# Optimization experiments

Hardware: AMD Instinct MI355X
Metric: run time of the kernel (lower is better)

Reference implementation:

```python
import jax, jax.numpy as jnp
import numpy as np

D_MODEL = 256
B, H, T = 4, 8, 2048
EPS = 1e-8


def _clinear(x_r, x_i, w_r, w_i, b_r, b_i):
    # complex matmul: (x_r + i x_i) @ (w_r + i w_i)^T + (b_r + i b_i)
    y_r = jnp.matmul(x_r, w_r.T) - jnp.matmul(x_i, w_i.T) + b_r
    y_i = jnp.matmul(x_i, w_r.T) + jnp.matmul(x_r, w_i.T) + b_i
    return y_r, y_i


def setup_inputs() -> dict:
    key = jax.random.key(0)
    ks = jax.random.split(key, 24)
    d = D_MODEL
    std = np.sqrt(2.0 / (d + d)) / np.sqrt(2.0)  # glorot-ish * 1/sqrt(2) as in _init_weights
    inp = {}
    inp['q_in_r'] = jax.random.normal(ks[0], (B, H, T, d), jnp.float32)
    inp['q_in_i'] = jax.random.normal(ks[1], (B, H, T, d), jnp.float32)
    inp['kv_in_r'] = jax.random.normal(ks[2], (B, H, T, d), jnp.float32)
    inp['kv_in_i'] = jax.random.normal(ks[3], (B, H, T, d), jnp.float32)
    i = 4
    for p in ['q', 'k', 'v', 'o']:
        inp[p + '_wr'] = std * jax.random.normal(ks[i], (d, d), jnp.float32); i += 1
        inp[p + '_wi'] = std * jax.random.normal(ks[i], (d, d), jnp.float32); i += 1
        inp[p + '_br'] = jnp.zeros((d,), jnp.float32)
        inp[p + '_bi'] = jnp.zeros((d,), jnp.float32)
    inp['gate_w'] = std * jax.random.normal(ks[i], (d, d), jnp.float32)
    inp['gate_b'] = jnp.zeros((d,), jnp.float32)
    return inp


def reference(q_in_r, q_in_i, kv_in_r, kv_in_i,
              q_wr, q_wi, q_br, q_bi,
              k_wr, k_wi, k_br, k_bi,
              v_wr, v_wi, v_br, v_bi,
              o_wr, o_wi, o_br, o_bi,
              gate_w, gate_b):
    D = q_in_r.shape[-1]
    q_r, q_i = _clinear(q_in_r, q_in_i, q_wr, q_wi, q_br, q_bi)
    k_r, k_i = _clinear(kv_in_r, kv_in_i, k_wr, k_wi, k_br, k_bi)
    v_r, v_i = _clinear(kv_in_r, kv_in_i, v_wr, v_wi, v_br, v_bi)
    scale = 1.0 / np.sqrt(D)
    # real part of complex inner product <q, k> (the module's dual-part score)
    scores = (jnp.einsum('bhqd,bhkd->bhqk', q_r, k_r)
              + jnp.einsum('bhqd,bhkd->bhqk', q_i, k_i)) * scale
    attn = jax.nn.softmax(scores, axis=-1)
    ctx_r = jnp.einsum('bhqk,bhkd->bhqd', attn, v_r)
    ctx_i = jnp.einsum('bhqk,bhkd->bhqd', attn, v_i)
    out_r, out_i = _clinear(ctx_r, ctx_i, o_wr, o_wi, o_br, o_bi)
    out_mag = jnp.sqrt(out_r ** 2 + out_i ** 2 + EPS)
    gate = jax.nn.sigmoid(jnp.matmul(out_mag, gate_w.T) + gate_b)
    return out_r * gate, out_i * gate
```

## Files before the change

kernel.cpp:

```cpp
#include <hip/hip_runtime.h>
#include <hip/hip_bf16.h>
#include <hip/hip_fp16.h>
#include <stdint.h>


#define TSEQ   2048
#define NHEADS 32
#define MTOT   65536
#define DDC    512
#define HCHUNK 8

typedef float    f32x4  __attribute__((ext_vector_type(4)));
typedef _Float16 f16x8  __attribute__((ext_vector_type(8)));
typedef uint16_t u16x4  __attribute__((ext_vector_type(4)));
typedef uint16_t u16x8  __attribute__((ext_vector_type(8)));

__device__ __forceinline__ uint16_t f2h(float f) {
  _Float16 h = (_Float16)f;
  return __builtin_bit_cast(uint16_t, h);
}
__device__ __forceinline__ float h2f(uint16_t u) {
  return (float)__builtin_bit_cast(_Float16, u);
}

__device__ __forceinline__ void gld16(const void* g, void* l) {
  __builtin_amdgcn_global_load_lds(
      (const __attribute__((address_space(1))) uint32_t*)g,
      (__attribute__((address_space(3))) uint32_t*)l, 16, 0, 0);
}

enum { EP_F16Z = 0, EP_PROJ = 1, EP_OUT = 2, EP_GATE = 3 };

template <int EP, int BM>
__global__ __launch_bounds__(512, (BM == 128) ? 4 : 2) void gemm_bt(
    const uint16_t* __restrict__ A, int lda, long zA,
    const uint16_t* __restrict__ B, int ldb, long zB,
    void* __restrict__ C, int ldc, long zC, uint16_t* __restrict__ CV,
    int K,
    const float* __restrict__ biasR, const float* __restrict__ biasI,
    float scale, float* __restrict__ outR, float* __restrict__ outI) {
  constexpr int MI    = BM / 32;
  constexpr int ASLAB = BM / 64;
  constexpr int ABUFE = BM * 64;
  constexpr int BUFE  = (BM + 256) * 64;
  constexpr int NLOAD = ASLAB + 4;
  __shared__ uint16_t lds[2 * BUFE];

  const int tid  = threadIdx.x;
  const int wave = tid >> 6;
  const int lane = tid & 63;
  const int wr   = (wave >> 2) * (BM / 2);
  const int wc   = (wave & 3) * 64;

  const int gx = gridDim.x, gy = gridDim.y;
  const int nwg = gx * gy * gridDim.z;
  const int lin = blockIdx.x + gx * (blockIdx.y + gy * blockIdx.z);
  const int cpx = nwg >> 3;
  const int swz = (lin & 7) * cpx + (lin >> 3);
  const int shx = __popc(gx - 1);
  const int shy = __popc(gy - 1);
  const int bx = swz & (gx - 1);
  const int by = (swz >> shx) & (gy - 1);
  const int bz = swz >> (shx + shy);

  const long tm = (long)by * BM;
  const long tn = (long)bx * 256;
  const uint16_t* Ab = A + (long)bz * zA;
  const uint16_t* Bb = B + (long)bz * zB;

  f32x4 acc[MI][4] = {};

  const int arow   = wave * 8 + (lane >> 3);
  const int schunk = (lane & 7) ^ (lane >> 3);

  const int fr   = lane & 15;
  const int quad = lane >> 4;
  const int sw   = fr & 7;
  const int ch0  = ((0 + quad) ^ sw) * 16;
  const int ch1  = ((4 + quad) ^ sw) * 16;

  const int nt = K >> 6;

  auto STAGE = [&](int buf, int t) {
    const long k0 = (long)t * 64 + schunk * 8;
    uint16_t* base = lds + buf * BUFE;
#pragma unroll
    for (int s = 0; s < ASLAB; ++s)
      gld16(Ab + (tm + s * 64 + arow) * (long)lda + k0,
            base + (s * 64 + wave * 8) * 64);
#pragma unroll
    for (int s = 0; s < 4; ++s)
      gld16(Bb + (tn + s * 64 + arow) * (long)ldb + k0,
            base + ABUFE + (s * 64 + wave * 8) * 64);
  };

  auto COMPUTE = [&](int buf) {
    const char* Abase = (const char*)(lds + buf * BUFE);
    const char* Bbase = Abase + 2 * ABUFE;
#pragma unroll
    for (int ks = 0; ks < 2; ++ks) {
      const int co = ks ? ch1 : ch0;
      f16x8 bf[4];
#pragma unroll
      for (int j = 0; j < 4; ++j)
        bf[j] = *(const f16x8*)(Bbase + (wc + j * 16 + fr) * 128 + co);
#pragma unroll
      for (int i = 0; i < MI; ++i) {
        const f16x8 af = *(const f16x8*)(Abase + (wr + i * 16 + fr) * 128 + co);
#pragma unroll
        for (int j = 0; j < 4; ++j)
          acc[i][j] = __builtin_amdgcn_mfma_f32_16x16x32_f16(af, bf[j], acc[i][j], 0, 0, 0);
      }
    }
  };

  STAGE(0, 0);
  int cur = 0;
  for (int t = 0; t < nt; ++t) {
    if (t + 1 < nt) {
      STAGE(cur ^ 1, t + 1);
      if constexpr (NLOAD == 8)      asm volatile("s_waitcnt vmcnt(8)" ::: "memory");
      else if constexpr (NLOAD == 6) asm volatile("s_waitcnt vmcnt(6)" ::: "memory");
      else                           asm volatile("s_waitcnt vmcnt(0)" ::: "memory");
    } else {
      asm volatile("s_waitcnt vmcnt(0)" ::: "memory");
    }
    __builtin_amdgcn_s_barrier();
    __builtin_amdgcn_sched_barrier(0);
    COMPUTE(cur);
    __builtin_amdgcn_sched_barrier(0);
    __builtin_amdgcn_s_barrier();
    __builtin_amdgcn_sched_barrier(0);
    cur ^= 1;
  }

  if constexpr (EP == EP_F16Z || EP == EP_PROJ) {
    __syncthreads();
    char* wbase = (char*)lds + wave * (BM * 64);
    uint16_t* Cp;
    int coff = 0;
    if constexpr (EP == EP_PROJ) {
      const bool vhalf = (CV != nullptr) && (tn >= 512);
      Cp = vhalf ? CV : (uint16_t*)C;
      coff = vhalf ? 512 : 0;
    } else {
      Cp = (uint16_t*)C + (long)bz * zC;
    }
#pragma unroll
    for (int i = 0; i < MI; ++i) {
#pragma unroll
      for (int j = 0; j < 4; ++j) {
#pragma unroll
        for (int r = 0; r < 4; ++r) {
          const int row = i * 16 + quad * 4 + r;
          int byte = row * 128 + (j * 16 + fr) * 2;
          byte ^= ((row >> 2) & 3) << 5;
          float v = acc[i][j][r];
          if constexpr (EP == EP_PROJ) {
            const int col = (int)tn + wc + j * 16 + fr;
            v += biasR[col];
          } else {
            v *= scale;
          }
          *(uint16_t*)(wbase + byte) = f2h(v);
        }
      }
    }
    asm volatile("s_waitcnt lgkmcnt(0)" ::: "memory");
    __builtin_amdgcn_sched_barrier(0);
#pragma unroll
    for (int it = 0; it < BM / 16; ++it) {
      const int row = it * 8 + (lane >> 3);
      const int c   = lane & 7;
      int byte = row * 128 + c * 16;
      byte ^= ((row >> 2) & 3) << 5;
      const u16x8 val = *(const u16x8*)(wbase + byte);
      const long grow = tm + wr + row;
      const int  gcol = (int)tn + wc + c * 8 - coff;
      *(u16x8*)(Cp + grow * (long)ldc + gcol) = val;
    }
  } else {
#pragma unroll
    for (int i = 0; i < MI; ++i) {
      const long row0 = tm + wr + i * 16 + quad * 4;
#pragma unroll
      for (int j = 0; j < 4; ++j) {
        const int col = (int)tn + wc + j * 16 + fr;
#pragma unroll
        for (int r = 0; r < 4; ++r) {
          float v = acc[i][j][r];
          const long rw = row0 + r;
          if constexpr (EP == EP_OUT) {
            if (col < 256) outR[rw * 256 + col]       = v + biasR[col];
            else           outI[rw * 256 + col - 256] = v + biasI[col - 256];
          } else {
            const float g = 1.0f / (1.0f + __expf(-(v + biasR[col])));
            const long o = rw * 256 + col;
            outR[o] *= g;
            outI[o] *= g;
          }
        }
      }
    }
  }
}

__global__ void pack_x(const float* __restrict__ xr, const float* __restrict__ xi,
                       uint16_t* __restrict__ out) {
  const long idx = (long)blockIdx.x * 256 + threadIdx.x;
  const long m  = idx >> 7;
  const int  c4 = (int)(idx & 127) << 2;
  const float* src = (c4 < 256) ? (xr + m * 256 + c4) : (xi + m * 256 + (c4 - 256));
  const float4 v = *(const float4*)src;
  u16x4 o = {f2h(v.x), f2h(v.y), f2h(v.z), f2h(v.w)};
  *(u16x4*)(out + m * 512 + c4) = o;
}

__global__ void pack_w(const float* __restrict__ wr, const float* __restrict__ wi,
                       uint16_t* __restrict__ out) {
  const int idx = blockIdx.x * 256 + threadIdx.x;
  const int j  = idx >> 7;
  const int c4 = (idx & 127) << 2;
  const float* src;
  float sgn = 1.f;
  if (j < 256) {
    if (c4 < 256) src = wr + j * 256 + c4;
    else { src = wi + j * 256 + (c4 - 256); sgn = -1.f; }
  } else {
    if (c4 < 256) src = wi + (j - 256) * 256 + c4;
    else          src = wr + (j - 256) * 256 + (c4 - 256);
  }
  const float4 v = *(const float4*)src;
  u16x4 o = {f2h(sgn * v.x), f2h(sgn * v.y), f2h(sgn * v.z), f2h(sgn * v.w)};
  *(u16x4*)(out + (long)j * 512 + c4) = o;
}

__global__ void pack_gw(const float* __restrict__ w, uint16_t* __restrict__ out) {
  const int idx = blockIdx.x * 256 + threadIdx.x;
  const float4 v = *(const float4*)(w + (long)idx * 4);
  u16x4 o = {f2h(v.x), f2h(v.y), f2h(v.z), f2h(v.w)};
  *(u16x4*)(out + (long)idx * 4) = o;
}

__global__ void pack_bias(const float* __restrict__ qbr, const float* __restrict__ qbi,
                          const float* __restrict__ kbr, const float* __restrict__ kbi,
                          const float* __restrict__ vbr, const float* __restrict__ vbi,
                          float* __restrict__ bq, float* __restrict__ bkv) {
  const int i = blockIdx.x * 256 + threadIdx.x;
  if (i < 256)       bq[i] = qbr[i];
  else if (i < 512)  bq[i] = qbi[i - 256];
  else if (i < 768)  bkv[i - 512] = kbr[i - 512];
  else if (i < 1024) bkv[i - 512] = kbi[i - 768];
  else if (i < 1280) bkv[i - 512] = vbr[i - 1024];
  else               bkv[i - 512] = vbi[i - 1280];
}

__global__ void transpose_v(const uint16_t* __restrict__ V, uint16_t* __restrict__ Vt) {
  __shared__ uint16_t t[32][33];
  const int h = blockIdx.z;
  const uint16_t* Vh = V + (long)h * TSEQ * DDC;
  uint16_t* Vth = Vt + (long)h * DDC * TSEQ;
  const int t0 = blockIdx.x * 32;
  const int n0 = blockIdx.y * 32;
  const int lx = threadIdx.x & 31, ly = threadIdx.x >> 5;
#pragma unroll
  for (int yy = ly; yy < 32; yy += 8)
    t[yy][lx] = Vh[(long)(t0 + yy) * DDC + n0 + lx];
  __syncthreads();
#pragma unroll
  for (int yy = ly; yy < 32; yy += 8)
    Vth[(long)(n0 + yy) * TSEQ + t0 + lx] = t[lx][yy];
}

__global__ __launch_bounds__(256) void softmax_rows(uint16_t* __restrict__ S) {
  const long row = blockIdx.x;
  uint16_t* p = S + row * 2048;
  const int tid = threadIdx.x;
  u16x8 raw = ((const u16x8*)p)[tid];
  float v[8];
#pragma unroll
  for (int j = 0; j < 8; ++j) v[j] = h2f(raw[j]);
  float m = v[0];
#pragma unroll
  for (int j = 1; j < 8; ++j) m = fmaxf(m, v[j]);
#pragma unroll
  for (int off = 32; off >= 1; off >>= 1) m = fmaxf(m, __shfl_xor(m, off));
  __shared__ float red[8];
  const int wave = tid >> 6, lane = tid & 63;
  if (lane == 0) red[wave] = m;
  __syncthreads();
  m = fmaxf(fmaxf(red[0], red[1]), fmaxf(red[2], red[3]));
  float s = 0.f;
#pragma unroll
  for (int j = 0; j < 8; ++j) { v[j] = __expf(v[j] - m); s += v[j]; }
#pragma unroll
  for (int off = 32; off >= 1; off >>= 1) s += __shfl_xor(s, off);
  if (lane == 0) red[4 + wave] = s;
  __syncthreads();
  s = red[4] + red[5] + red[6] + red[7];
  const float inv = 1.0f / s;
  u16x8 o;
#pragma unroll
  for (int j = 0; j < 8; ++j) o[j] = f2h(v[j] * inv);
  ((u16x8*)p)[tid] = o;
}

__global__ void mag_kernel(const float* __restrict__ R, const float* __restrict__ I,
                           uint16_t* __restrict__ mag) {
  const long i = ((long)blockIdx.x * 256 + threadIdx.x) * 4;
  const float4 r  = *(const float4*)(R + i);
  const float4 im = *(const float4*)(I + i);
  u16x4 o = {f2h(sqrtf(r.x * r.x + im.x * im.x + 1e-8f)),
             f2h(sqrtf(r.y * r.y + im.y * im.y + 1e-8f)),
             f2h(sqrtf(r.z * r.z + im.z * im.z + 1e-8f)),
             f2h(sqrtf(r.w * r.w + im.w * im.w + 1e-8f))};
  *(u16x4*)(mag + i) = o;
}

extern "C" void kernel_launch(void* const* d_in, const int* in_sizes, int n_in,
                              void* d_out, int out_size, void* d_ws, size_t ws_size,
                              hipStream_t stream) {
  const float* q_in_r  = (const float*)d_in[0];
  const float* q_in_i  = (const float*)d_in[1];
  const float* kv_in_r = (const float*)d_in[2];
  const float* kv_in_i = (const float*)d_in[3];
  const float* q_wr = (const float*)d_in[4];
  const float* q_wi = (const float*)d_in[5];
  const float* q_br = (const float*)d_in[6];
  const float* q_bi = (const float*)d_in[7];
  const float* k_wr = (const float*)d_in[8];
  const float* k_wi = (const float*)d_in[9];
  const float* k_br = (const float*)d_in[10];
  const float* k_bi = (const float*)d_in[11];
  const float* v_wr = (const float*)d_in[12];
  const float* v_wi = (const float*)d_in[13];
  const float* v_br = (const float*)d_in[14];
  const float* v_bi = (const float*)d_in[15];
  const float* o_wr = (const float*)d_in[16];
  const float* o_wi = (const float*)d_in[17];
  const float* o_br = (const float*)d_in[18];
  const float* o_bi = (const float*)d_in[19];
  const float* gate_w = (const float*)d_in[20];
  const float* gate_b = (const float*)d_in[21];

  unsigned char* w = (unsigned char*)d_ws;
  const size_t MAT16 = (size_t)MTOT * DDC * 2;
  size_t off = 0;
  uint16_t* R1 = (uint16_t*)(w + off); off += MAT16;
  uint16_t* R2 = (uint16_t*)(w + off); off += MAT16;
  uint16_t* R3 = (uint16_t*)(w + off); off += MAT16;
  uint16_t* R4 = (uint16_t*)(w + off); off += MAT16;
  uint16_t* R5 = (uint16_t*)(w + off); off += MAT16;
  uint16_t* Wq = (uint16_t*)(w + off); off += 512 * 512 * 2;
  uint16_t* Wk = (uint16_t*)(w + off); off += 512 * 512 * 2;
  uint16_t* Wv = (uint16_t*)(w + off); off += 512 * 512 * 2;
  uint16_t* Wo = (uint16_t*)(w + off); off += 512 * 512 * 2;
  uint16_t* Gw = (uint16_t*)(w + off); off += 256 * 256 * 2;
  float*    Bq  = (float*)(w + off);   off += 512 * 4;
  float*    Bkv = (float*)(w + off);   off += 1024 * 4;

  uint16_t* Xq  = R1; uint16_t* Vt  = R1;
  uint16_t* Xkv = R2; uint16_t* Ctx = R2;
  uint16_t* Qm  = R3; uint16_t* Mag = R3;
  uint16_t* Km  = R4;
  uint16_t* Vm  = R5; uint16_t* Sc  = R5;

  float* outR = (float*)d_out;
  float* outI = (float*)d_out + (long)MTOT * 256;

  pack_x<<<32768, 256, 0, stream>>>(q_in_r, q_in_i, Xq);
  pack_x<<<32768, 256, 0, stream>>>(kv_in_r, kv_in_i, Xkv);
  pack_w<<<256, 256, 0, stream>>>(q_wr, q_wi, Wq);
  pack_w<<<256, 256, 0, stream>>>(k_wr, k_wi, Wk);
  pack_w<<<256, 256, 0, stream>>>(v_wr, v_wi, Wv);
  pack_w<<<256, 256, 0, stream>>>(o_wr, o_wi, Wo);
  pack_gw<<<64, 256, 0, stream>>>(gate_w, Gw);
  pack_bias<<<6, 256, 0, stream>>>(q_br, q_bi, k_br, k_bi, v_br, v_bi, Bq, Bkv);

  gemm_bt<EP_PROJ, 256><<<dim3(2, 256, 1), 512, 0, stream>>>(
      Xq, 512, 0, Wq, 512, 0, Qm, 512, 0, nullptr, 512, Bq, nullptr, 1.f,
      nullptr, nullptr);
  gemm_bt<EP_PROJ, 256><<<dim3(4, 256, 1), 512, 0, stream>>>(
      Xkv, 512, 0, Wk, 512, 0, Km, 512, 0, Vm, 512, Bkv, nullptr, 1.f,
      nullptr, nullptr);
  transpose_v<<<dim3(64, 16, 32), 256, 0, stream>>>(Vm, Vt);

  for (int c = 0; c < NHEADS / HCHUNK; ++c) {
    const long ho = (long)c * HCHUNK;
    gemm_bt<EP_F16Z, 256><<<dim3(8, 8, HCHUNK), 512, 0, stream>>>(
        Qm + ho * TSEQ * DDC, 512, (long)TSEQ * DDC,
        Km + ho * TSEQ * DDC, 512, (long)TSEQ * DDC,
        Sc, TSEQ, (long)TSEQ * TSEQ, nullptr, 512,
        nullptr, nullptr, 0.0625f, nullptr, nullptr);
    softmax_rows<<<HCHUNK * TSEQ, 256, 0, stream>>>(Sc);
    gemm_bt<EP_F16Z, 128><<<dim3(2, 16, HCHUNK), 512, 0, stream>>>(
        Sc, TSEQ, (long)TSEQ * TSEQ,
        Vt + ho * DDC * TSEQ, TSEQ, (long)DDC * TSEQ,
        Ctx + ho * TSEQ * DDC, 512, (long)TSEQ * DDC, nullptr, 2048,
        nullptr, nullptr, 1.f, nullptr, nullptr);
  }

  gemm_bt<EP_OUT, 256><<<dim3(2, 256, 1), 512, 0, stream>>>(
      Ctx, 512, 0, Wo, 512, 0, nullptr, 0, 0, nullptr, 512,
      o_br, o_bi, 1.f, outR, outI);

  mag_kernel<<<16384, 256, 0, stream>>>(outR, outI, Mag);

  gemm_bt<EP_GATE, 256><<<dim3(1, 256, 1), 512, 0, stream>>>(
      Mag, 256, 0, Gw, 256, 0, nullptr, 0, 0, nullptr, 256,
      gate_b, nullptr, 1.f, outR, outI);
}
```

Before: 1.119 ms.

## Shrink GEMM tiles to 128x128x32 with four-wave workgroups

Replaces the templated 256/128-row by 256-column tile GEMM with a fixed 128x128 tile, a K step of 32, and 256-thread workgroups. The LDS swizzle, staging loads, wait counts and all launch grids are rebuilt to match. The goal is more workgroups and higher occupancy, at the cost of less operand reuse per tile and twice as many barrier-separated K iterations.

```diff
diff --git a/kernel.cpp b/kernel.cpp
--- a/kernel.cpp
+++ b/kernel.cpp
@@ -31,26 +31,23 @@
 
 enum { EP_F16Z = 0, EP_PROJ = 1, EP_OUT = 2, EP_GATE = 3 };
 
-template <int EP, int BM>
-__global__ __launch_bounds__(512, (BM == 128) ? 4 : 2) void gemm_bt(
+template <int EP>
+__global__ __launch_bounds__(256, 4) void gemm_bt(
     const uint16_t* __restrict__ A, int lda, long zA,
     const uint16_t* __restrict__ B, int ldb, long zB,
     void* __restrict__ C, int ldc, long zC, uint16_t* __restrict__ CV,
     int K,
     const float* __restrict__ biasR, const float* __restrict__ biasI,
     float scale, float* __restrict__ outR, float* __restrict__ outI) {
-  constexpr int MI    = BM / 32;
-  constexpr int ASLAB = BM / 64;
-  constexpr int ABUFE = BM * 64;
-  constexpr int BUFE  = (BM + 256) * 64;
-  constexpr int NLOAD = ASLAB + 4;
+  constexpr int ABUFE = 128 * 32;
+  constexpr int BUFE  = 2 * ABUFE;
   __shared__ uint16_t lds[2 * BUFE];
 
   const int tid  = threadIdx.x;
   const int wave = tid >> 6;
   const int lane = tid & 63;
-  const int wr   = (wave >> 2) * (BM / 2);
-  const int wc   = (wave & 3) * 64;
+  const int wr   = (wave >> 1) * 64;
+  const int wc   = (wave & 1) * 64;
 
   const int gx = gridDim.x, gy = gridDim.y;
   const int nwg = gx * gy * gridDim.z;
@@ -63,54 +60,48 @@
   const int by = (swz >> shx) & (gy - 1);
   const int bz = swz >> (shx + shy);
 
-  const long tm = (long)by * BM;
-  const long tn = (long)bx * 256;
+  const long tm = (long)by * 128;
+  const long tn = (long)bx * 128;
   const uint16_t* Ab = A + (long)bz * zA;
   const uint16_t* Bb = B + (long)bz * zB;
 
-  f32x4 acc[MI][4] = {};
-
-  const int arow   = wave * 8 + (lane >> 3);
-  const int schunk = (lane & 7) ^ (lane >> 3);
+  f32x4 acc[4][4] = {};
+
+  const int srow   = wave * 16 + (lane >> 2);
+  const int schunk = (lane & 3) ^ ((lane >> 2) & 3);
 
   const int fr   = lane & 15;
   const int quad = lane >> 4;
-  const int sw   = fr & 7;
-  const int ch0  = ((0 + quad) ^ sw) * 16;
-  const int ch1  = ((4 + quad) ^ sw) * 16;
-
-  const int nt = K >> 6;
+  const int co   = ((quad ^ (fr & 3)) << 4);
+
+  const int nt = K >> 5;
 
   auto STAGE = [&](int buf, int t) {
-    const long k0 = (long)t * 64 + schunk * 8;
+    const long k0 = (long)t * 32 + schunk * 8;
     uint16_t* base = lds + buf * BUFE;
 #pragma unroll
-    for (int s = 0; s < ASLAB; ++s)
-      gld16(Ab + (tm + s * 64 + arow) * (long)lda + k0,
-            base + (s * 64 + wave * 8) * 64);
-#pragma unroll
-    for (int s = 0; s < 4; ++s)
-      gld16(Bb + (tn + s * 64 + arow) * (long)ldb + k0,
-            base + ABUFE + (s * 64 + wave * 8) * 64);
+    for (int s = 0; s < 2; ++s)
+      gld16(Ab + (tm + s * 64 + srow) * (long)lda + k0,
+            base + (s * 64 + wave * 16) * 32);
+#pragma unroll
+    for (int s = 0; s < 2; ++s)
+      gld16(Bb + (tn + s * 64 + srow) * (long)ldb + k0,
+            base + ABUFE + (s * 64 + wave * 16) * 32);
   };
 
   auto COMPUTE = [&](int buf) {
     const char* Abase = (const char*)(lds + buf * BUFE);
-    const char* Bbase = Abase + 2 * ABUFE;
-#pragma unroll
-    for (int ks = 0; ks < 2; ++ks) {
-      const int co = ks ? ch1 : ch0;
-      f16x8 bf[4];
+    const char* Bbase = (const char*)(lds + buf * BUFE + ABUFE);
+    f16x8 bf[4];
+#pragma unroll
+    for (int j = 0; j < 4; ++j)
+      bf[j] = *(const f16x8*)(Bbase + (wc + j * 16 + fr) * 64 + co);
+#pragma unroll
+    for (int i = 0; i < 4; ++i) {
+      const f16x8 af = *(const f16x8*)(Abase + (wr + i * 16 + fr) * 64 + co);
 #pragma unroll
       for (int j = 0; j < 4; ++j)
-        bf[j] = *(const f16x8*)(Bbase + (wc + j * 16 + fr) * 128 + co);
-#pragma unroll
-      for (int i = 0; i < MI; ++i) {
-        const f16x8 af = *(const f16x8*)(Abase + (wr + i * 16 + fr) * 128 + co);
-#pragma unroll
-        for (int j = 0; j < 4; ++j)
-          acc[i][j] = __builtin_amdgcn_mfma_f32_16x16x32_f16(af, bf[j], acc[i][j], 0, 0, 0);
-      }
+        acc[i][j] = __builtin_amdgcn_mfma_f32_16x16x32_f16(af, bf[j], acc[i][j], 0, 0, 0);
     }
   };
 
@@ -119,9 +110,7 @@
   for (int t = 0; t < nt; ++t) {
     if (t + 1 < nt) {
       STAGE(cur ^ 1, t + 1);
-      if constexpr (NLOAD == 8)      asm volatile("s_waitcnt vmcnt(8)" ::: "memory");
-      else if constexpr (NLOAD == 6) asm volatile("s_waitcnt vmcnt(6)" ::: "memory");
-      else                           asm volatile("s_waitcnt vmcnt(0)" ::: "memory");
+      asm volatile("s_waitcnt vmcnt(4)" ::: "memory");
     } else {
       asm volatile("s_waitcnt vmcnt(0)" ::: "memory");
     }
@@ -136,7 +125,7 @@
 
   if constexpr (EP == EP_F16Z || EP == EP_PROJ) {
     __syncthreads();
-    char* wbase = (char*)lds + wave * (BM * 64);
+    char* wbase = (char*)lds + wave * 8192;
     uint16_t* Cp;
     int coff = 0;
     if constexpr (EP == EP_PROJ) {
@@ -146,13 +135,14 @@
     } else {
       Cp = (uint16_t*)C + (long)bz * zC;
     }
-#pragma unroll
-    for (int i = 0; i < MI; ++i) {
+    const int iquad = lane >> 4;
+#pragma unroll
+    for (int i = 0; i < 4; ++i) {
 #pragma unroll
       for (int j = 0; j < 4; ++j) {
 #pragma unroll
         for (int r = 0; r < 4; ++r) {
-          const int row = i * 16 + quad * 4 + r;
+          const int row = i * 16 + iquad * 4 + r;
           int byte = row * 128 + (j * 16 + fr) * 2;
           byte ^= ((row >> 2) & 3) << 5;
           float v = acc[i][j][r];
@@ -169,7 +159,7 @@
     asm volatile("s_waitcnt lgkmcnt(0)" ::: "memory");
     __builtin_amdgcn_sched_barrier(0);
 #pragma unroll
-    for (int it = 0; it < BM / 16; ++it) {
+    for (int it = 0; it < 8; ++it) {
       const int row = it * 8 + (lane >> 3);
       const int c   = lane & 7;
       int byte = row * 128 + c * 16;
@@ -180,9 +170,10 @@
       *(u16x8*)(Cp + grow * (long)ldc + gcol) = val;
     }
   } else {
-#pragma unroll
-    for (int i = 0; i < MI; ++i) {
-      const long row0 = tm + wr + i * 16 + quad * 4;
+    const int iquad = lane >> 4;
+#pragma unroll
+    for (int i = 0; i < 4; ++i) {
+      const long row0 = tm + wr + i * 16 + iquad * 4;
 #pragma unroll
       for (int j = 0; j < 4; ++j) {
         const int col = (int)tn + wc + j * 16 + fr;
@@ -377,36 +368,36 @@
   pack_gw<<<64, 256, 0, stream>>>(gate_w, Gw);
   pack_bias<<<6, 256, 0, stream>>>(q_br, q_bi, k_br, k_bi, v_br, v_bi, Bq, Bkv);
 
-  gemm_bt<EP_PROJ, 256><<<dim3(2, 256, 1), 512, 0, stream>>>(
+  gemm_bt<EP_PROJ><<<dim3(4, 512, 1), 256, 0, stream>>>(
       Xq, 512, 0, Wq, 512, 0, Qm, 512, 0, nullptr, 512, Bq, nullptr, 1.f,
       nullptr, nullptr);
-  gemm_bt<EP_PROJ, 256><<<dim3(4, 256, 1), 512, 0, stream>>>(
+  gemm_bt<EP_PROJ><<<dim3(8, 512, 1), 256, 0, stream>>>(
       Xkv, 512, 0, Wk, 512, 0, Km, 512, 0, Vm, 512, Bkv, nullptr, 1.f,
       nullptr, nullptr);
   transpose_v<<<dim3(64, 16, 32), 256, 0, stream>>>(Vm, Vt);
 
   for (int c = 0; c < NHEADS / HCHUNK; ++c) {
     const long ho = (long)c * HCHUNK;
-    gemm_bt<EP_F16Z, 256><<<dim3(8, 8, HCHUNK), 512, 0, stream>>>(
+    gemm_bt<EP_F16Z><<<dim3(16, 16, HCHUNK), 256, 0, stream>>>(
         Qm + ho * TSEQ * DDC, 512, (long)TSEQ * DDC,
         Km + ho * TSEQ * DDC, 512, (long)TSEQ * DDC,
         Sc, TSEQ, (long)TSEQ * TSEQ, nullptr, 512,
         nullptr, nullptr, 0.0625f, nullptr, nullptr);
     softmax_rows<<<HCHUNK * TSEQ, 256, 0, stream>>>(Sc);
-    gemm_bt<EP_F16Z, 128><<<dim3(2, 16, HCHUNK), 512, 0, stream>>>(
+    gemm_bt<EP_F16Z><<<dim3(4, 16, HCHUNK), 256, 0, stream>>>(
         Sc, TSEQ, (long)TSEQ * TSEQ,
         Vt + ho * DDC * TSEQ, TSEQ, (long)DDC * TSEQ,
         Ctx + ho * TSEQ * DDC, 512, (long)TSEQ * DDC, nullptr, 2048,
         nullptr, nullptr, 1.f, nullptr, nullptr);
   }
 
-  gemm_bt<EP_OUT, 256><<<dim3(2, 256, 1), 512, 0, stream>>>(
+  gemm_bt<EP_OUT><<<dim3(4, 512, 1), 256, 0, stream>>>(
       Ctx, 512, 0, Wo, 512, 0, nullptr, 0, 0, nullptr, 512,
       o_br, o_bi, 1.f, outR, outI);
 
   mag_kernel<<<16384, 256, 0, stream>>>(outR, outI, Mag);
 
-  gemm_bt<EP_GATE, 256><<<dim3(1, 256, 1), 512, 0, stream>>>(
+  gemm_bt<EP_GATE><<<dim3(2, 512, 1), 256, 0, stream>>>(
       Mag, 256, 0, Gw, 256, 0, nullptr, 0, 0, nullptr, 256,
       gate_b, nullptr, 1.f, outR, outI);
 }
```

Result: slower. 1.159 ms (+3.6%).
